# Kernel optimization log

Hardware: AMD Instinct MI355X
Metric: run time of the kernel (lower is better)

The kernel has to match this reference:

```python
import jax, jax.numpy as jnp
import numpy as np

N_NODES = 250000
N_EDGES = 4000000
NUM_FEATURES = 1
HIDDEN_DIM = 16
NUM_CLASSES = 4


def setup_inputs() -> dict:
    key = jax.random.key(0)
    ks = jax.random.split(key, 8)
    x = jax.random.normal(ks[0], (N_NODES, NUM_FEATURES), dtype=jnp.float32)
    edge_index = jax.random.randint(ks[1], (2, N_EDGES), 0, N_NODES, dtype=jnp.int64)
    # GCNConv weights: lin has no bias; bias added after aggregation
    W1 = jax.random.normal(ks[2], (NUM_FEATURES, HIDDEN_DIM), dtype=jnp.float32) * 0.5
    b1 = jax.random.normal(ks[3], (HIDDEN_DIM,), dtype=jnp.float32) * 0.1
    W2 = jax.random.normal(ks[4], (HIDDEN_DIM, HIDDEN_DIM), dtype=jnp.float32) * 0.25
    b2 = jax.random.normal(ks[5], (HIDDEN_DIM,), dtype=jnp.float32) * 0.1
    Wfc = jax.random.normal(ks[6], (HIDDEN_DIM, NUM_CLASSES), dtype=jnp.float32) * 0.25
    bfc = jax.random.normal(ks[7], (NUM_CLASSES,), dtype=jnp.float32) * 0.1
    return {"x": x, "edge_index": edge_index, "W1": W1, "b1": b1,
            "W2": W2, "b2": b2, "Wfc": Wfc, "bfc": bfc}


def _gcn_conv(x, row, col, norm, W, b, n):
    # x: [N, F_in]; row/col: [E'] (source/target incl self-loops); norm: [E']
    h = x @ W                                  # [N, F_out]
    msg = h[row] * norm[:, None]               # gather + scale, [E', F_out]
    out = jax.ops.segment_sum(msg, col, num_segments=n)  # scatter-add, [N, F_out]
    return out + b


def reference(x, edge_index, W1, b1, W2, b2, Wfc, bfc):
    n = x.shape[0]
    loops = jnp.arange(n, dtype=edge_index.dtype)
    row = jnp.concatenate([edge_index[0], loops])  # source nodes + self-loops
    col = jnp.concatenate([edge_index[1], loops])  # target nodes + self-loops
    # symmetric normalization: deg computed over targets (incl self-loops)
    deg = jax.ops.segment_sum(jnp.ones(col.shape, x.dtype), col, num_segments=n)
    dinv = jnp.where(deg > 0, jax.lax.rsqrt(deg), 0.0)
    norm = dinv[row] * dinv[col]                   # [E']
    h = jax.nn.relu(_gcn_conv(x, row, col, norm, W1, b1, n))
    h = jax.nn.relu(_gcn_conv(h, row, col, norm, W2, b2, n))
    return h @ Wfc + bfc
```

## Files before the change

kernel.cpp:

```cpp
#include <hip/hip_runtime.h>
#include <math.h>

#define HD 16
#define NC 4
#define BSH 8
#define BSZ 256
#define NSB 64
#define SBSH 12
#define NB1 1024
#define CAPB 128
#define CAP2S 384
#define NFB 1024
#define NIV 17
#define STR 35
#define AGT 512
#define SMASK 0x3FFFFu

typedef unsigned uint4e __attribute__((ext_vector_type(4)));
typedef float    float4e __attribute__((ext_vector_type(4)));

__global__ void k_thr(const float* __restrict__ W1, const float* __restrict__ b1,
                      float* __restrict__ ts, int* __restrict__ splits,
                      int* __restrict__ signs) {
    if (threadIdx.x != 0 || blockIdx.x != 0) return;
    float tt[HD], s[HD];
    for (int f = 0; f < HD; ++f) {
        float w = W1[f];
        tt[f] = (w != 0.0f) ? (-b1[f] / w) : INFINITY;
        s[f] = tt[f];
    }
    for (int i = 1; i < HD; ++i) {
        float key = s[i]; int j = i - 1;
        while (j >= 0 && s[j] > key) { s[j + 1] = s[j]; --j; }
        s[j + 1] = key;
    }
    for (int f = 0; f < HD; ++f) ts[f] = s[f];
    for (int f = 0; f < HD; ++f) {
        float w = W1[f];
        if (w == 0.0f) { signs[f] = 0; splits[f] = 0; continue; }
        int c = 0;
        for (int g = 0; g < HD; ++g) c += (s[g] < tt[f]) ? 1 : 0;
        splits[f] = c + 1;
        signs[f] = (w > 0.0f) ? 1 : -1;
    }
}

__global__ void k_part1(const int* __restrict__ row, const int* __restrict__ col,
                        int* __restrict__ cnts1, unsigned* __restrict__ bins1,
                        int E, int CHK) {
    __shared__ int ofs[NSB];
    int t = threadIdx.x;
    int b = blockIdx.x;
    int cb = b * CHK;
    int ce = min(E, cb + CHK);
    int n = ce - cb; if (n < 0) n = 0;
    if (t < NSB) ofs[t] = 0;
    __syncthreads();
    int nv = n >> 2;
    const uint4* col4 = reinterpret_cast<const uint4*>(col + cb);
    const uint4* row4 = reinterpret_cast<const uint4*>(row + cb);
    for (int i = t; i < nv; i += 256) {
        uint4 c4 = col4[i];
        uint4 r4 = row4[i];
        {
            unsigned c = c4.x; int sb = (int)(c >> SBSH);
            int pos = atomicAdd(&ofs[sb], 1);
            if (pos < CAPB)
                bins1[((((size_t)sb << 10) | b) << 7) + pos] = r4.x | ((c & 4095u) << 18);
        }
        {
            unsigned c = c4.y; int sb = (int)(c >> SBSH);
            int pos = atomicAdd(&ofs[sb], 1);
            if (pos < CAPB)
                bins1[((((size_t)sb << 10) | b) << 7) + pos] = r4.y | ((c & 4095u) << 18);
        }
        {
            unsigned c = c4.z; int sb = (int)(c >> SBSH);
            int pos = atomicAdd(&ofs[sb], 1);
            if (pos < CAPB)
                bins1[((((size_t)sb << 10) | b) << 7) + pos] = r4.z | ((c & 4095u) << 18);
        }
        {
            unsigned c = c4.w; int sb = (int)(c >> SBSH);
            int pos = atomicAdd(&ofs[sb], 1);
            if (pos < CAPB)
                bins1[((((size_t)sb << 10) | b) << 7) + pos] = r4.w | ((c & 4095u) << 18);
        }
    }
    for (int e = (nv << 2) + t; e < n; e += 256) {
        unsigned c = (unsigned)col[cb + e];
        int sb = (int)(c >> SBSH);
        int pos = atomicAdd(&ofs[sb], 1);
        if (pos < CAPB)
            bins1[((((size_t)sb << 10) | b) << 7) + pos] =
                (unsigned)row[cb + e] | ((c & 4095u) << 18);
    }
    __syncthreads();
    if (t < NSB) cnts1[t * NB1 + b] = ofs[t];
}

__global__ void k_part2(const unsigned* __restrict__ bins1, const int* __restrict__ cnts1,
                        int* __restrict__ cnts2, unsigned* __restrict__ bins2) {
    __shared__ int ofs[16];
    __shared__ int cnt[64];
    int t = threadIdx.x;
    int sb = blockIdx.x >> 4;
    int sp = blockIdx.x & 15;
    if (t < 64) {
        int c = cnts1[sb * NB1 + sp * 64 + t];
        cnt[t] = (c > CAPB) ? CAPB : c;
    }
    if (t < 16) ofs[t] = 0;
    __syncthreads();
    const unsigned* base = bins1 + ((((size_t)sb << 10) | (sp * 64)) << 7);
    for (int j = t << 2; j < 64 * CAPB; j += 1024) {
        uint4 rr = *reinterpret_cast<const uint4*>(base + j);
        int cs = cnt[j >> 7];
        int p0 = j & 127;
        #pragma unroll
        for (int q = 0; q < 4; ++q) {
            if (p0 + q < cs) {
                unsigned rec = (q == 0) ? rr.x : (q == 1) ? rr.y : (q == 2) ? rr.z : rr.w;
                int fl = rec >> 26;
                int pos = atomicAdd(&ofs[fl], 1);
                if (pos < CAP2S)
                    bins2[((size_t)(sb * 16 + fl) * 16 + sp) * CAP2S + pos] =
                        (rec & SMASK) | (((rec >> 18) & 255u) << 18);
            }
        }
    }
    __syncthreads();
    if (t < 16) {
        int c = ofs[t];
        cnts2[(sb * 16 + t) * 16 + sp] = (c > CAP2S) ? CAP2S : c;
    }
}

__global__ void k_degdx(const unsigned* __restrict__ bins, const int* __restrict__ cnts2,
                        const float* __restrict__ x,
                        float* __restrict__ dinv, float* __restrict__ dx, int N) {
    __shared__ int cnt[BSZ];
    __shared__ int cs_[16];
    __shared__ int gb[17];
    int t = threadIdx.x, b = blockIdx.x;
    cnt[t] = 0;
    if (t < 16) {
        int c = cnts2[b * 16 + t];
        cs_[t] = (c > CAP2S) ? CAP2S : c;
    }
    __syncthreads();
    if (t == 0) {
        int a = 0;
        for (int s2 = 0; s2 < 16; ++s2) { gb[s2] = a; a += (cs_[s2] + 3) >> 2; }
        gb[16] = a;
    }
    __syncthreads();
    int gtot = gb[16];
    const unsigned* bb = bins + (size_t)b * 16 * CAP2S;
    for (int g = t; g < gtot; g += 256) {
        int seg = 0;
        #pragma unroll
        for (int s2 = 1; s2 < 16; ++s2) seg += (g >= gb[s2]);
        int pos = (g - gb[seg]) << 2;
        int cs = cs_[seg];
        uint4e rr = __builtin_nontemporal_load(
            reinterpret_cast<const uint4e*>(bb + seg * CAP2S + pos));
        if (pos + 0 < cs) atomicAdd(&cnt[rr[0] >> 18], 1);
        if (pos + 1 < cs) atomicAdd(&cnt[rr[1] >> 18], 1);
        if (pos + 2 < cs) atomicAdd(&cnt[rr[2] >> 18], 1);
        if (pos + 3 < cs) atomicAdd(&cnt[rr[3] >> 18], 1);
    }
    __syncthreads();
    int node = (b << BSH) + t;
    if (node < N) {
        float d = rsqrtf((float)(cnt[t] + 1));
        dinv[node] = d;
        dx[node] = d * x[node];
    }
}

__global__ void k_s1(const unsigned* __restrict__ bins, const int* __restrict__ cnts2,
                     const float* __restrict__ dinv, const float* __restrict__ dx,
                     const float* __restrict__ ts,
                     float2* __restrict__ gpq, int N) {
    __shared__ float sacc[BSZ];
    __shared__ int cs_[16];
    __shared__ int gb[17];
    int t = threadIdx.x, b = blockIdx.x;
    sacc[t] = 0.0f;
    if (t < 16) {
        int c = cnts2[b * 16 + t];
        cs_[t] = (c > CAP2S) ? CAP2S : c;
    }
    __syncthreads();
    if (t == 0) {
        int a = 0;
        for (int s2 = 0; s2 < 16; ++s2) { gb[s2] = a; a += (cs_[s2] + 3) >> 2; }
        gb[16] = a;
    }
    __syncthreads();
    int gtot = gb[16];
    const unsigned* bb = bins + (size_t)b * 16 * CAP2S;
    for (int g = t; g < gtot; g += 256) {
        int seg = 0;
        #pragma unroll
        for (int s2 = 1; s2 < 16; ++s2) seg += (g >= gb[s2]);
        int pos = (g - gb[seg]) << 2;
        int cs = cs_[seg];
        uint4e rr = __builtin_nontemporal_load(
            reinterpret_cast<const uint4e*>(bb + seg * CAP2S + pos));
        if (pos + 0 < cs) atomicAdd(&sacc[rr[0] >> 18], dx[rr[0] & SMASK]);
        if (pos + 1 < cs) atomicAdd(&sacc[rr[1] >> 18], dx[rr[1] & SMASK]);
        if (pos + 2 < cs) atomicAdd(&sacc[rr[2] >> 18], dx[rr[2] & SMASK]);
        if (pos + 3 < cs) atomicAdd(&sacc[rr[3] >> 18], dx[rr[3] & SMASK]);
    }
    __syncthreads();
    int node = (b << BSH) + t;
    if (node < N) {
        float d = dinv[node];
        float S = d * (sacc[t] + dx[node]);
        int k = 0;
        #pragma unroll
        for (int g = 0; g < HD; ++g) k += (S > ts[g]);
        unsigned dq = (__float_as_uint(d) & ~31u) | (unsigned)k;
        gpq[node] = make_float2(d * S, __uint_as_float(dq));
    }
}

__global__ void __launch_bounds__(AGT, 1)
k_agg(const unsigned* __restrict__ bins, const int* __restrict__ cnts2,
      const float2* __restrict__ gpq, const float* __restrict__ dinv,
      const int* __restrict__ splits, const int* __restrict__ signs,
      const float* __restrict__ W1, const float* __restrict__ b1,
      const float* __restrict__ W2, const float* __restrict__ b2,
      const float* __restrict__ Wfc, const float* __restrict__ bfc,
      float* __restrict__ out, int N) {
    __shared__ float acc[BSZ * STR];
    __shared__ int cs_[16];
    __shared__ int gb[17];
    int t = threadIdx.x, b = blockIdx.x;
    for (int i = t; i < BSZ * STR; i += AGT) acc[i] = 0.0f;
    if (t < 16) {
        int c = cnts2[b * 16 + t];
        cs_[t] = (c > CAP2S) ? CAP2S : c;
    }
    __syncthreads();
    if (t == 0) {
        int a = 0;
        for (int s2 = 0; s2 < 16; ++s2) { gb[s2] = a; a += (cs_[s2] + 3) >> 2; }
        gb[16] = a;
    }
    __syncthreads();
    int gtot = gb[16];
    const unsigned* bb = bins + (size_t)b * 16 * CAP2S;
    for (int g = t; g < gtot; g += AGT) {
        int seg = 0;
        #pragma unroll
        for (int s2 = 1; s2 < 16; ++s2) seg += (g >= gb[s2]);
        int pos = (g - gb[seg]) << 2;
        int cs = cs_[seg];
        uint4e rr = __builtin_nontemporal_load(
            reinterpret_cast<const uint4e*>(bb + seg * CAP2S + pos));
        if (pos + 0 < cs) {
            float2 p = gpq[rr[0] & SMASK];
            float* a = &acc[(int)(rr[0] >> 18) * STR + 2 * (int)(__float_as_uint(p.y) & 31u)];
            atomicAdd(a, p.x); atomicAdd(a + 1, p.y);
        }
        if (pos + 1 < cs) {
            float2 p = gpq[rr[1] & SMASK];
            float* a = &acc[(int)(rr[1] >> 18) * STR + 2 * (int)(__float_as_uint(p.y) & 31u)];
            atomicAdd(a, p.x); atomicAdd(a + 1, p.y);
        }
        if (pos + 2 < cs) {
            float2 p = gpq[rr[2] & SMASK];
            float* a = &acc[(int)(rr[2] >> 18) * STR + 2 * (int)(__float_as_uint(p.y) & 31u)];
            atomicAdd(a, p.x); atomicAdd(a + 1, p.y);
        }
        if (pos + 3 < cs) {
            float2 p = gpq[rr[3] & SMASK];
            float* a = &acc[(int)(rr[3] >> 18) * STR + 2 * (int)(__float_as_uint(p.y) & 31u)];
            atomicAdd(a, p.x); atomicAdd(a + 1, p.y);
        }
    }
    __syncthreads();

    int node = (b << BSH) + t;
    if (t >= BSZ || node >= N) return;
    float Ppre[NIV + 1], Qpre[NIV + 1];
    float pp = 0.0f, qq = 0.0f;
    #pragma unroll
    for (int mm = 0; mm < NIV; ++mm) {
        Ppre[mm] = pp; Qpre[mm] = qq;
        pp += acc[t * STR + 2 * mm];
        qq += acc[t * STR + 2 * mm + 1];
    }
    Ppre[NIV] = pp; Qpre[NIV] = qq;

    float2 pq = gpq[node];
    float di = dinv[node];
    float si = pq.x / di;
    float aggv[HD];
    #pragma unroll
    for (int f = 0; f < HD; ++f) {
        int sp = splits[f], sg = signs[f];
        float w = W1[f], bb2 = b1[f];
        float A, B;
        if (sg > 0)      { A = pp - Ppre[sp]; B = qq - Qpre[sp]; }
        else if (sg < 0) { A = Ppre[sp];      B = Qpre[sp]; }
        else             { A = 0.0f;          B = (bb2 > 0.0f) ? qq : 0.0f; }
        float selfh = fmaxf(fmaf(w, si, bb2), 0.0f);
        aggv[f] = di * (fmaf(w, A, bb2 * B) + di * selfh);
    }
    float o0 = bfc[0], o1 = bfc[1], o2 = bfc[2], o3 = bfc[3];
    #pragma unroll
    for (int f2 = 0; f2 < HD; ++f2) {
        float h = b2[f2];
        #pragma unroll
        for (int k = 0; k < HD; ++k) h = fmaf(aggv[k], W2[k * HD + f2], h);
        h = fmaxf(h, 0.0f);
        o0 = fmaf(h, Wfc[f2 * NC + 0], o0);
        o1 = fmaf(h, Wfc[f2 * NC + 1], o1);
        o2 = fmaf(h, Wfc[f2 * NC + 2], o2);
        o3 = fmaf(h, Wfc[f2 * NC + 3], o3);
    }
    float4e ov = { o0, o1, o2, o3 };
    __builtin_nontemporal_store(ov, reinterpret_cast<float4e*>(out) + node);
}

extern "C" void kernel_launch(void* const* d_in, const int* in_sizes, int n_in,
                              void* d_out, int out_size, void* d_ws, size_t ws_size,
                              hipStream_t stream) {
    const float* x   = (const float*)d_in[0];
    const int*   ei  = (const int*)d_in[1];
    const float* W1  = (const float*)d_in[2];
    const float* b1  = (const float*)d_in[3];
    const float* W2  = (const float*)d_in[4];
    const float* b2  = (const float*)d_in[5];
    const float* Wfc = (const float*)d_in[6];
    const float* bfc = (const float*)d_in[7];
    float* out = (float*)d_out;

    const int N = in_sizes[0];
    const int E = in_sizes[1] / 2;
    const int* row = ei;
    const int* col = ei + E;

    char* ws = (char*)d_ws;
    size_t off = 0;
    unsigned* bins1 = (unsigned*)(ws + off); off += (size_t)NSB * NB1 * CAPB * 4;
    unsigned* bins2 = (unsigned*)(ws + off); off += (size_t)NFB * 16 * CAP2S * 4;
    int*    cnts1 = (int*)(ws + off);    off += (size_t)NSB * NB1 * 4;
    int*    cnts2 = (int*)(ws + off);    off += (size_t)NFB * 16 * 4;
    float*  dinv  = (float*)(ws + off);  off += (size_t)N * 4;
    float*  dx    = (float*)(ws + off);  off += (size_t)N * 4;
    float2* gpq   = (float2*)(ws + off); off += (size_t)N * 8;
    float*  ts    = (float*)(ws + off);  off += 64;
    int*    splits= (int*)(ws + off);    off += 64;
    int*    signs = (int*)(ws + off);    off += 64;

    const int B = 256;
    k_thr<<<1, 64, 0, stream>>>(W1, b1, ts, splits, signs);
    int CHK = (E + NB1 - 1) / NB1;
    CHK = (CHK + 3) & ~3;
    k_part1<<<NB1, B, 0, stream>>>(row, col, cnts1, bins1, E, CHK);
    k_part2<<<NSB * 16, B, 0, stream>>>(bins1, cnts1, cnts2, bins2);
    k_degdx<<<NFB, B, 0, stream>>>(bins2, cnts2, x, dinv, dx, N);
    k_s1<<<NFB, B, 0, stream>>>(bins2, cnts2, dinv, dx, ts, gpq, N);
    k_agg<<<NFB, AGT, 0, stream>>>(bins2, cnts2, gpq, dinv, splits, signs,
                                   W1, b1, W2, b2, Wfc, bfc, out, N);
}
```

Baseline: 209.2 us.

## Pack P/Q accumulators into fixed-point 64-bit LDS atomics

Replaces the two float LDS atomicAdds per edge with a single 64-bit integer atomicAdd. P and Q are converted to 2^19-scaled fixed point, with P biased by 16*Q so it stays non-negative, and both halves are packed into one word and unpacked after accumulation. This halves the number of LDS atomics and replaces float atomics with integer ones. The cost is quantization error and a risk of overflow into the high half or of negative values if the bias is not large enough. It also drops the padded stride, which may bring back bank conflicts.

```diff
diff --git a/kernel.cpp b/kernel.cpp
--- a/kernel.cpp
+++ b/kernel.cpp
@@ -12,8 +12,10 @@
 #define CAP2S 384
 #define NFB 1024
 #define NIV 17
-#define STR 35
 #define AGT 512
+#define FPS2 524288.0f
+#define IFPS2 (1.0f/524288.0f)
+#define CBIAS 16.0f
 #define SMASK 0x3FFFFu
 
 typedef unsigned uint4e __attribute__((ext_vector_type(4)));
@@ -235,11 +237,11 @@
       const float* __restrict__ W2, const float* __restrict__ b2,
       const float* __restrict__ Wfc, const float* __restrict__ bfc,
       float* __restrict__ out, int N) {
-    __shared__ float acc[BSZ * STR];
+    __shared__ unsigned long long acc[BSZ * NIV];
     __shared__ int cs_[16];
     __shared__ int gb[17];
     int t = threadIdx.x, b = blockIdx.x;
-    for (int i = t; i < BSZ * STR; i += AGT) acc[i] = 0.0f;
+    for (int i = t; i < BSZ * NIV; i += AGT) acc[i] = 0ull;
     if (t < 16) {
         int c = cnts2[b * 16 + t];
         cs_[t] = (c > CAP2S) ? CAP2S : c;
@@ -261,25 +263,19 @@
         int cs = cs_[seg];
         uint4e rr = __builtin_nontemporal_load(
             reinterpret_cast<const uint4e*>(bb + seg * CAP2S + pos));
-        if (pos + 0 < cs) {
-            float2 p = gpq[rr[0] & SMASK];
-            float* a = &acc[(int)(rr[0] >> 18) * STR + 2 * (int)(__float_as_uint(p.y) & 31u)];
-            atomicAdd(a, p.x); atomicAdd(a + 1, p.y);
-        }
-        if (pos + 1 < cs) {
-            float2 p = gpq[rr[1] & SMASK];
-            float* a = &acc[(int)(rr[1] >> 18) * STR + 2 * (int)(__float_as_uint(p.y) & 31u)];
-            atomicAdd(a, p.x); atomicAdd(a + 1, p.y);
-        }
-        if (pos + 2 < cs) {
-            float2 p = gpq[rr[2] & SMASK];
-            float* a = &acc[(int)(rr[2] >> 18) * STR + 2 * (int)(__float_as_uint(p.y) & 31u)];
-            atomicAdd(a, p.x); atomicAdd(a + 1, p.y);
-        }
-        if (pos + 3 < cs) {
-            float2 p = gpq[rr[3] & SMASK];
-            float* a = &acc[(int)(rr[3] >> 18) * STR + 2 * (int)(__float_as_uint(p.y) & 31u)];
-            atomicAdd(a, p.x); atomicAdd(a + 1, p.y);
+        #pragma unroll
+        for (int q = 0; q < 4; ++q) {
+            if (pos + q < cs) {
+                unsigned rec = rr[q];
+                float2 p = gpq[rec & SMASK];
+                int k = (int)(__float_as_uint(p.y) & 31u);
+                float dq = p.y;
+                float vP = fmaf(CBIAS, dq, p.x);
+                unsigned uP = (unsigned)(vP * FPS2 + 0.5f);
+                unsigned uQ = (unsigned)(dq * FPS2 + 0.5f);
+                unsigned long long pk = ((unsigned long long)uP << 32) | (unsigned long long)uQ;
+                atomicAdd(&acc[(int)(rec >> 18) * NIV + k], pk);
+            }
         }
     }
     __syncthreads();
@@ -291,8 +287,11 @@
     #pragma unroll
     for (int mm = 0; mm < NIV; ++mm) {
         Ppre[mm] = pp; Qpre[mm] = qq;
-        pp += acc[t * STR + 2 * mm];
-        qq += acc[t * STR + 2 * mm + 1];
+        unsigned long long v = acc[t * NIV + mm];
+        float Q = (float)(unsigned)(v & 0xFFFFFFFFull) * IFPS2;
+        float Ph = (float)(unsigned)(v >> 32) * IFPS2;
+        pp += fmaf(-CBIAS, Q, Ph);
+        qq += Q;
     }
     Ppre[NIV] = pp; Qpre[NIV] = qq;
 
```

Result: faster. 191.2 us (-8.6%).
